# Performance work log

Hardware: AMD Instinct MI355X
Metric: run time of the kernel (lower is better)

The kernel has to match this reference:

```python
import jax, jax.numpy as jnp
import numpy as np

B, S, HID = 2, 2048, 1024
H, KVH = 16, 4           # query heads, kv heads
D = HID // H             # head_dim = 64
G = H // KVH             # group size (n_rep) = 4


def setup_inputs() -> dict:
    key = jax.random.key(0)
    ks = jax.random.split(key, 6)
    x = jax.random.normal(ks[0], (B, S, HID), dtype=jnp.float32)
    # RoPE tables: [S, D], standard theta=10000
    inv_freq = 1.0 / (10000.0 ** (jnp.arange(0, D, 2, dtype=jnp.float32) / D))
    freqs = jnp.arange(S, dtype=jnp.float32)[:, None] * inv_freq[None, :]  # [S, D/2]
    emb = jnp.concatenate([freqs, freqs], axis=-1)  # [S, D]
    cos, sin = jnp.cos(emb), jnp.sin(emb)
    scale = 0.02
    wq = jax.random.normal(ks[1], (HID, H * D), dtype=jnp.float32) * scale
    wk = jax.random.normal(ks[2], (HID, KVH * D), dtype=jnp.float32) * scale
    wv = jax.random.normal(ks[3], (HID, KVH * D), dtype=jnp.float32) * scale
    wo = jax.random.normal(ks[4], (H * D, HID), dtype=jnp.float32) * scale
    return {"x": x, "cos": cos, "sin": sin, "wq": wq, "wk": wk, "wv": wv, "wo": wo}


def _rotate_half(t):
    h = t.shape[-1] // 2
    return jnp.concatenate([-t[..., h:], t[..., :h]], axis=-1)


def reference(x, cos, sin, wq, wk, wv, wo):
    b, s, _ = x.shape
    q = (x @ wq).reshape(b, s, H, D)
    k = (x @ wk).reshape(b, s, KVH, D)
    v = (x @ wv).reshape(b, s, KVH, D)
    # RoPE (cos/sin broadcast over heads, unsqueeze_dim=1 -> [S,1,D])
    c = cos[:s, None, :]
    sn = sin[:s, None, :]
    q = q * c + _rotate_half(q) * sn
    k = k * c + _rotate_half(k) * sn
    # GQA attention without materializing repeated K/V: group q heads by kv head
    qg = q.reshape(b, s, KVH, G, D)
    scores = jnp.einsum('bqkgd,bskd->bkgqs', qg, k) / jnp.sqrt(jnp.asarray(D, q.dtype))
    causal = jnp.tril(jnp.ones((s, s), dtype=bool))  # [S_q, S_k]
    scores = jnp.where(causal[None, None, None, :, :], scores, -jnp.inf)
    p = jax.nn.softmax(scores, axis=-1)
    out = jnp.einsum('bkgqs,bskd->bqkgd', p, v).reshape(b, s, H * D)
    return out @ wo
```

## Files before the change

kernel.cpp:

```cpp
#include <hip/hip_runtime.h>
#include <hip/hip_bf16.h>


typedef short bfx8 __attribute__((ext_vector_type(8)));
typedef float fx4  __attribute__((ext_vector_type(4)));
typedef float fx16 __attribute__((ext_vector_type(16)));
typedef unsigned int ux4 __attribute__((ext_vector_type(4)));

#define DEV __device__ __forceinline__
#define ALPHA 0.18033688011112042f

DEV void load_lds16(const void* g, void* l) {
  __builtin_amdgcn_global_load_lds(
      (const __attribute__((address_space(1))) unsigned int*)g,
      (__attribute__((address_space(3))) unsigned int*)l, 16, 0, 0);
}

DEV unsigned short f2bf(float f) {
  unsigned int x = __builtin_bit_cast(unsigned int, f);
  unsigned int r = (x + 0x7fffu + ((x >> 16) & 1u)) >> 16;
  return (unsigned short)r;
}
DEV float bf2f(unsigned short u) {
  unsigned int x = ((unsigned int)u) << 16;
  return __builtin_bit_cast(float, x);
}
DEV float exp2_fast(float x) { float r; asm("v_exp_f32 %0, %1" : "=v"(r) : "v"(x)); return r; }
DEV unsigned cvtpk(float lo, float hi) {
  unsigned r; asm("v_cvt_pk_bf16_f32 %0, %1, %2" : "=v"(r) : "v"(lo), "v"(hi)); return r;
}


__global__ __launch_bounds__(256) void cvt_x_kernel(const float* __restrict__ x,
                                                    unsigned short* __restrict__ out) {
  int i = (blockIdx.x * 256 + threadIdx.x) * 8;
  fx4 a = *(const fx4*)(x + i);
  fx4 b = *(const fx4*)(x + i + 4);
  bfx8 r;
  r[0] = (short)f2bf(a[0]); r[1] = (short)f2bf(a[1]);
  r[2] = (short)f2bf(a[2]); r[3] = (short)f2bf(a[3]);
  r[4] = (short)f2bf(b[0]); r[5] = (short)f2bf(b[1]);
  r[6] = (short)f2bf(b[2]); r[7] = (short)f2bf(b[3]);
  *(bfx8*)(out + i) = r;
}


__global__ __launch_bounds__(256) void twqkv_kernel(const float* __restrict__ wq,
                                                    const float* __restrict__ wk,
                                                    const float* __restrict__ wv,
                                                    unsigned short* __restrict__ out) {
  __shared__ float tile[64 * 65];
  const int r0 = blockIdx.x * 64;
  const int c0 = blockIdx.y * 64;
  const float* src; int ncols, rofs;
  if (r0 < 1024)      { src = wq; ncols = 1024; rofs = r0; }
  else if (r0 < 1280) { src = wk; ncols = 256;  rofs = r0 - 1024; }
  else                { src = wv; ncols = 256;  rofs = r0 - 1280; }
  const int t = threadIdx.x;
#pragma unroll
  for (int p = 0; p < 4; ++p) {
    int idx = p * 256 + t;
    int cc = idx >> 4, q4 = idx & 15;
    fx4 v = *(const fx4*)(src + (size_t)(c0 + cc) * ncols + rofs + q4 * 4);
#pragma unroll
    for (int i = 0; i < 4; ++i) tile[(q4 * 4 + i) * 65 + cc] = v[i];
  }
  __syncthreads();
#pragma unroll
  for (int p = 0; p < 2; ++p) {
    int idx = p * 256 + t;
    int rr = idx >> 3, c8 = idx & 7;
    bfx8 v8;
#pragma unroll
    for (int i = 0; i < 8; ++i) v8[i] = (short)f2bf(tile[rr * 65 + c8 * 8 + i]);
    *(bfx8*)(out + (size_t)(r0 + rr) * 1024 + c0 + c8 * 8) = v8;
  }
}

__global__ __launch_bounds__(256) void two_kernel(const float* __restrict__ wo,
                                                  unsigned short* __restrict__ out) {
  __shared__ float tile[64 * 65];
  const int r0 = blockIdx.x * 64, c0 = blockIdx.y * 64;
  const int t = threadIdx.x;
#pragma unroll
  for (int p = 0; p < 4; ++p) {
    int idx = p * 256 + t;
    int cc = idx >> 4, q4 = idx & 15;
    fx4 v = *(const fx4*)(wo + (size_t)(c0 + cc) * 1024 + r0 + q4 * 4);
#pragma unroll
    for (int i = 0; i < 4; ++i) tile[(q4 * 4 + i) * 65 + cc] = v[i];
  }
  __syncthreads();
#pragma unroll
  for (int p = 0; p < 2; ++p) {
    int idx = p * 256 + t;
    int rr = idx >> 3, c8 = idx & 7;
    bfx8 v8;
#pragma unroll
    for (int i = 0; i < 8; ++i) v8[i] = (short)f2bf(tile[rr * 65 + c8 * 8 + i]);
    *(bfx8*)(out + (size_t)(r0 + rr) * 1024 + c0 + c8 * 8) = v8;
  }
}


__global__ __launch_bounds__(256) void vt_kernel(const unsigned short* __restrict__ qkv,
                                                 unsigned short* __restrict__ vT) {
  __shared__ __align__(16) unsigned short tile[64][72];
  const int sc = blockIdx.x;
  const int kvh = blockIdx.y, b = blockIdx.z;
  const int t = threadIdx.x;
  const unsigned short* src = qkv + ((size_t)b * 2048 + sc * 64) * 1536 + 1280 + kvh * 64;
#pragma unroll
  for (int p = 0; p < 2; ++p) {
    int idx = p * 256 + t;
    int row = idx >> 3, c = idx & 7;
    *(bfx8*)(&tile[row][c * 8]) = *(const bfx8*)(src + (size_t)row * 1536 + c * 8);
  }
  __syncthreads();
  unsigned short* dst = vT + ((size_t)(b * 4 + kvh) * 64) * 2048 + sc * 64;
#pragma unroll
  for (int p = 0; p < 2; ++p) {
    int idx = p * 256 + t;
    int d = idx >> 3, c = idx & 7;
    bfx8 v;
#pragma unroll
    for (int i = 0; i < 8; ++i) v[i] = (short)tile[c * 8 + i][d];
    *(bfx8*)(dst + (size_t)d * 2048 + c * 8) = v;
  }
}


template <bool OUT_BF16, bool FUSE_ROPE>
__global__ __launch_bounds__(256) void gemm_bt_kernel(const unsigned short* __restrict__ A,
                                                      const unsigned short* __restrict__ Bt,
                                                      void* __restrict__ Cp,
                                                      int M, int N, int K, int ldc,
                                                      const float* __restrict__ ct,
                                                      const float* __restrict__ st) {
  __shared__ __align__(16) unsigned short As[128 * 32];
  __shared__ __align__(16) unsigned short Bs[128 * 32];
  const int t = threadIdx.x;
  const int l = t & 63;
  const int w = t >> 6;
  const int wm = (w >> 1) * 64, wn = (w & 1) * 64;
  const int bm = blockIdx.x, bn = blockIdx.y;
  fx4 acc[4][4] = {};

  const int ra = t >> 2;
  const int ca = t & 3;

  for (int kt = 0; kt < K; kt += 32) {
    __syncthreads();
#pragma unroll
    for (int p = 0; p < 2; ++p) {
      int rr = ra + p * 64;
      int gca = ((ca ^ ((rr >> 1) & 3)) * 8);
      load_lds16(A + (size_t)(bm * 128 + rr) * K + kt + gca, (char*)As + p * 4096 + t * 16);
      load_lds16(Bt + (size_t)(bn * 128 + rr) * K + kt + gca, (char*)Bs + p * 4096 + t * 16);
    }
    __syncthreads();

    bfx8 af[4], bfr[4];
#pragma unroll
    for (int mi = 0; mi < 4; ++mi) {
      int row = wm + mi * 16 + (l & 15);
      int ch = (l >> 4) ^ ((row >> 1) & 3);
      af[mi] = *(const bfx8*)(As + row * 32 + ch * 8);
      int rowb = wn + mi * 16 + (l & 15);
      int chb = (l >> 4) ^ ((rowb >> 1) & 3);
      bfr[mi] = *(const bfx8*)(Bs + rowb * 32 + chb * 8);
    }
#pragma unroll
    for (int mi = 0; mi < 4; ++mi)
#pragma unroll
      for (int ni = 0; ni < 4; ++ni)
        acc[mi][ni] = __builtin_amdgcn_mfma_f32_16x16x32_bf16(af[mi], bfr[ni], acc[mi][ni], 0, 0, 0);
  }

  const int colbase = bn * 128 + wn;
  if (FUSE_ROPE && colbase < 1280) {
    const float qsc = (colbase < 1024) ? ALPHA : 1.0f;
    unsigned short* Cb = (unsigned short*)Cp;
#pragma unroll
    for (int mi = 0; mi < 4; ++mi) {
      int row0 = bm * 128 + wm + mi * 16 + (l >> 4) * 4;
#pragma unroll
      for (int r = 0; r < 4; ++r) {
        int row = row0 + r, s = row & 2047;
#pragma unroll
        for (int ni = 0; ni < 2; ++ni) {
          int d = ni * 16 + (l & 15);
          float c = ct[s * 64 + d], sn = st[s * 64 + d];
          float x0 = acc[mi][ni][r], x1 = acc[mi][ni + 2][r];
          Cb[(size_t)row * ldc + colbase + d]      = f2bf((x0 * c - x1 * sn) * qsc);
          Cb[(size_t)row * ldc + colbase + d + 32] = f2bf((x1 * c + x0 * sn) * qsc);
        }
      }
    }
  } else {
#pragma unroll
    for (int mi = 0; mi < 4; ++mi) {
      int row0 = bm * 128 + wm + mi * 16 + (l >> 4) * 4;
#pragma unroll
      for (int ni = 0; ni < 4; ++ni) {
        int col = colbase + ni * 16 + (l & 15);
#pragma unroll
        for (int r = 0; r < 4; ++r) {
          if (OUT_BF16)
            ((unsigned short*)Cp)[(size_t)(row0 + r) * ldc + col] = f2bf(acc[mi][ni][r]);
          else
            ((float*)Cp)[(size_t)(row0 + r) * ldc + col] = acc[mi][ni][r];
        }
      }
    }
  }
}


struct Frag { bfx8 kf[4]; bfx8 vf[4]; };

__global__ __launch_bounds__(64) void attn_kernel(const unsigned short* __restrict__ qkv,
                                                  const unsigned short* __restrict__ vT,
                                                  unsigned short* __restrict__ out) {
  __shared__ unsigned Ost[32 * 33];
  const int fid = blockIdx.x;
  const int pid = fid & 31;
  const int uu = fid >> 5;
  const int head = uu & 15, b = uu >> 4;
  const int kvh = head >> 2;
  const int l = threadIdx.x, q5 = l & 31, h = l >> 5;
  const size_t bbase = (size_t)b * 2048;
  const unsigned short* base = qkv + bbase * 1536;
  const unsigned short* kptr = base + 1024 + kvh * 64 + (size_t)q5 * 1536 + 8 * h;
  const unsigned short* vptr = vT + ((size_t)(b * 4 + kvh) * 64 + q5) * 2048 + 8 * h;

  Frag fA, fB;

#define LOADF(F, KB) do {                                                        \
    const unsigned short* kq = kptr + (size_t)(KB) * (32 * 1536);                \
    F.kf[0] = *(const bfx8*)(kq);                                                \
    F.kf[1] = *(const bfx8*)(kq + 16);                                           \
    F.kf[2] = *(const bfx8*)(kq + 32);                                           \
    F.kf[3] = *(const bfx8*)(kq + 48);                                           \
    const unsigned short* vq = vptr + (KB) * 32;                                 \
    F.vf[0] = *(const bfx8*)(vq);                                                \
    F.vf[1] = *(const bfx8*)(vq + 32 * 2048);                                    \
    F.vf[2] = *(const bfx8*)(vq + 16);                                           \
    F.vf[3] = *(const bfx8*)(vq + 16 + 32 * 2048);                               \
  } while (0)

#define STEP(F, KB) do {                                                         \
    fx16 s = {};                                                                 \
    s = __builtin_amdgcn_mfma_f32_32x32x16_bf16(F.kf[0], qf[0], s, 0, 0, 0);     \
    s = __builtin_amdgcn_mfma_f32_32x32x16_bf16(F.kf[1], qf[1], s, 0, 0, 0);     \
    s = __builtin_amdgcn_mfma_f32_32x32x16_bf16(F.kf[2], qf[2], s, 0, 0, 0);     \
    s = __builtin_amdgcn_mfma_f32_32x32x16_bf16(F.kf[3], qf[3], s, 0, 0, 0);     \
    if ((KB) == Tp) {                                                            \
      _Pragma("unroll")                                                          \
      for (int r = 0; r < 16; ++r) {                                             \
        int kr = (r & 3) + 8 * (r >> 2) + 4 * h;                                 \
        if (kr > q5) s[r] = -1e30f;                                              \
      }                                                                          \
    }                                                                            \
    float pmax = s[0];                                                           \
    _Pragma("unroll")                                                            \
    for (int r = 1; r < 16; ++r) pmax = fmaxf(pmax, s[r]);                       \
    pmax = fmaxf(pmax, __shfl_xor(pmax, 32, 64));                                \
    if (!__all(pmax <= mrun + 8.0f)) {                                           \
      float mnew = fmaxf(mrun, pmax);                                            \
      float corr = exp2_fast(mrun - mnew);                                       \
      mrun = mnew;                                                               \
      lrun *= corr;                                                              \
      o[0] *= corr; o[1] *= corr;                                                \
    }                                                                            \
    float lt = 0.f;                                                              \
    _Pragma("unroll")                                                            \
    for (int r = 0; r < 16; ++r) { float pv = exp2_fast(s[r] - mrun); s[r] = pv; lt += pv; } \
    lt += __shfl_xor(lt, 32, 64);                                                \
    lrun += lt;                                                                  \
    unsigned U[8];                                                               \
    _Pragma("unroll")                                                            \
    for (int k8 = 0; k8 < 8; ++k8) U[k8] = cvtpk(s[2 * k8], s[2 * k8 + 1]);      \
    _Pragma("unroll")                                                            \
    for (int kc = 0; kc < 2; ++kc) {                                             \
      unsigned send0 = h ? U[4 * kc] : U[4 * kc + 2];                            \
      unsigned send1 = h ? U[4 * kc + 1] : U[4 * kc + 3];                        \
      unsigned r0 = (unsigned)__shfl_xor((int)send0, 32, 64);                    \
      unsigned r1 = (unsigned)__shfl_xor((int)send1, 32, 64);                    \
      unsigned k0 = h ? U[4 * kc + 2] : U[4 * kc];                               \
      unsigned k1 = h ? U[4 * kc + 3] : U[4 * kc + 1];                           \
      ux4 fr;                                                                    \
      fr[0] = h ? r0 : k0; fr[1] = h ? r1 : k1;                                  \
      fr[2] = h ? k0 : r0; fr[3] = h ? k1 : r1;                                  \
      bfx8 pf = __builtin_bit_cast(bfx8, fr);                                    \
      o[0] = __builtin_amdgcn_mfma_f32_32x32x16_bf16(F.vf[kc * 2], pf, o[0], 0, 0, 0);     \
      o[1] = __builtin_amdgcn_mfma_f32_32x32x16_bf16(F.vf[kc * 2 + 1], pf, o[1], 0, 0, 0); \
    }                                                                            \
  } while (0)

#pragma unroll 1
  for (int sel = 0; sel < 2; ++sel) {
    const int Tp = sel ? (63 - pid) : pid;
    const int q0 = Tp * 32;
    const int nkb = Tp + 1;

    bfx8 qf[4];
#pragma unroll
    for (int dd = 0; dd < 4; ++dd)
      qf[dd] = *(const bfx8*)(base + (size_t)(q0 + q5) * 1536 + head * 64 + dd * 16 + 8 * h);

    fx16 o[2] = {};
    float mrun = -1e30f, lrun = 0.f;

    LOADF(fA, 0);
    int kb = 0;
    while (true) {
      if (kb + 1 < nkb) LOADF(fB, kb + 1);
      STEP(fA, kb);
      ++kb; if (kb >= nkb) break;
      if (kb + 1 < nkb) LOADF(fA, kb + 1);
      STEP(fB, kb);
      ++kb; if (kb >= nkb) break;
    }

    __syncthreads();
    float inv = 1.0f / lrun;
#pragma unroll
    for (int dt = 0; dt < 2; ++dt)
#pragma unroll
      for (int rp = 0; rp < 8; ++rp) {
        int r = 2 * rp;
        float a = o[dt][r] * inv, bb = o[dt][r + 1] * inv;
        int d = 32 * dt + (r & 3) + 8 * (r >> 2) + 4 * h;
        Ost[q5 * 33 + (d >> 1)] = cvtpk(a, bb);
      }
    __syncthreads();
    {
      int rr = l >> 1, half = l & 1;
      const unsigned* src = Ost + rr * 33 + half * 16;
      unsigned short* dst = out + (bbase + q0 + rr) * 1024 + head * 64 + half * 32;
#pragma unroll
      for (int u2 = 0; u2 < 4; ++u2) {
        ux4 v4;
        v4[0] = src[4 * u2]; v4[1] = src[4 * u2 + 1];
        v4[2] = src[4 * u2 + 2]; v4[3] = src[4 * u2 + 3];
        *(ux4*)(dst + u2 * 8) = v4;
      }
    }
  }
#undef LOADF
#undef STEP
}


extern "C" void kernel_launch(void* const* d_in, const int* in_sizes, int n_in,
                              void* d_out, int out_size, void* d_ws, size_t ws_size,
                              hipStream_t stream) {
  const float* x    = (const float*)d_in[0];
  const float* cosb = (const float*)d_in[1];
  const float* sinb = (const float*)d_in[2];
  const float* wq   = (const float*)d_in[3];
  const float* wk   = (const float*)d_in[4];
  const float* wv   = (const float*)d_in[5];
  const float* wo   = (const float*)d_in[6];
  float* out = (float*)d_out;

  char* ws = (char*)d_ws;
  unsigned short* xb    = (unsigned short*)ws;
  unsigned short* attn  = (unsigned short*)ws;
  unsigned short* wqkvT = (unsigned short*)(ws + 8388608);
  unsigned short* vT    = (unsigned short*)(ws + 8388608);
  unsigned short* woT   = (unsigned short*)(ws + 11534336);
  unsigned short* qkv   = (unsigned short*)(ws + 13631488);

  cvt_x_kernel<<<2048, 256, 0, stream>>>(x, xb);
  twqkv_kernel<<<dim3(24, 16), 256, 0, stream>>>(wq, wk, wv, wqkvT);
  two_kernel<<<dim3(16, 16), 256, 0, stream>>>(wo, woT);
  gemm_bt_kernel<true, true><<<dim3(32, 12), 256, 0, stream>>>(xb, wqkvT, qkv, 4096, 1536, 1024, 1536, cosb, sinb);
  vt_kernel<<<dim3(32, 4, 2), 256, 0, stream>>>(qkv, vT);
  attn_kernel<<<1024, 64, 0, stream>>>(qkv, vT, attn);
  gemm_bt_kernel<false, false><<<dim3(32, 8), 256, 0, stream>>>(attn, woT, out, 4096, 1024, 1024, 1024, nullptr, nullptr);
}
```

Before: 210.2 us.

## Split attention KV loop across two waves and merge weight-transpose kernels

The attention kernel now runs two wavefronts per block. Each wave processes alternating key blocks with triple-buffered fragment loads, and the partial softmax states (max, sum, output) are merged through shared memory before the output is written. This is meant to double the parallelism per query tile and shorten the serial KV loop, at the cost of extra LDS traffic, barriers and a combine step. Separately, the Q/K/V and O weight transpose kernels are fused into one launch to save a kernel launch.

```diff
diff --git a/kernel.cpp b/kernel.cpp
--- a/kernel.cpp
+++ b/kernel.cpp
@@ -45,17 +45,24 @@
 }
 
 
-__global__ __launch_bounds__(256) void twqkv_kernel(const float* __restrict__ wq,
-                                                    const float* __restrict__ wk,
-                                                    const float* __restrict__ wv,
-                                                    unsigned short* __restrict__ out) {
+__global__ __launch_bounds__(256) void tw_kernel(const float* __restrict__ wq,
+                                                 const float* __restrict__ wk,
+                                                 const float* __restrict__ wv,
+                                                 const float* __restrict__ wo,
+                                                 unsigned short* __restrict__ wqkvT,
+                                                 unsigned short* __restrict__ woT) {
   __shared__ float tile[64 * 65];
-  const int r0 = blockIdx.x * 64;
+  const int bx = blockIdx.x;
   const int c0 = blockIdx.y * 64;
-  const float* src; int ncols, rofs;
-  if (r0 < 1024)      { src = wq; ncols = 1024; rofs = r0; }
-  else if (r0 < 1280) { src = wk; ncols = 256;  rofs = r0 - 1024; }
-  else                { src = wv; ncols = 256;  rofs = r0 - 1280; }
+  const float* src; int ncols, rofs, r0; unsigned short* dst;
+  if (bx < 24) {
+    r0 = bx * 64; dst = wqkvT;
+    if (r0 < 1024)      { src = wq; ncols = 1024; rofs = r0; }
+    else if (r0 < 1280) { src = wk; ncols = 256;  rofs = r0 - 1024; }
+    else                { src = wv; ncols = 256;  rofs = r0 - 1280; }
+  } else {
+    r0 = (bx - 24) * 64; dst = woT; src = wo; ncols = 1024; rofs = r0;
+  }
   const int t = threadIdx.x;
 #pragma unroll
   for (int p = 0; p < 4; ++p) {
@@ -73,32 +80,7 @@
     bfx8 v8;
 #pragma unroll
     for (int i = 0; i < 8; ++i) v8[i] = (short)f2bf(tile[rr * 65 + c8 * 8 + i]);
-    *(bfx8*)(out + (size_t)(r0 + rr) * 1024 + c0 + c8 * 8) = v8;
-  }
-}
-
-__global__ __launch_bounds__(256) void two_kernel(const float* __restrict__ wo,
-                                                  unsigned short* __restrict__ out) {
-  __shared__ float tile[64 * 65];
-  const int r0 = blockIdx.x * 64, c0 = blockIdx.y * 64;
-  const int t = threadIdx.x;
-#pragma unroll
-  for (int p = 0; p < 4; ++p) {
-    int idx = p * 256 + t;
-    int cc = idx >> 4, q4 = idx & 15;
-    fx4 v = *(const fx4*)(wo + (size_t)(c0 + cc) * 1024 + r0 + q4 * 4);
-#pragma unroll
-    for (int i = 0; i < 4; ++i) tile[(q4 * 4 + i) * 65 + cc] = v[i];
-  }
-  __syncthreads();
-#pragma unroll
-  for (int p = 0; p < 2; ++p) {
-    int idx = p * 256 + t;
-    int rr = idx >> 3, c8 = idx & 7;
-    bfx8 v8;
-#pragma unroll
-    for (int i = 0; i < 8; ++i) v8[i] = (short)f2bf(tile[rr * 65 + c8 * 8 + i]);
-    *(bfx8*)(out + (size_t)(r0 + rr) * 1024 + c0 + c8 * 8) = v8;
+    *(bfx8*)(dst + (size_t)(r0 + rr) * 1024 + c0 + c8 * 8) = v8;
   }
 }
 
@@ -219,22 +201,25 @@
 
 struct Frag { bfx8 kf[4]; bfx8 vf[4]; };
 
-__global__ __launch_bounds__(64) void attn_kernel(const unsigned short* __restrict__ qkv,
-                                                  const unsigned short* __restrict__ vT,
-                                                  unsigned short* __restrict__ out) {
+__global__ __launch_bounds__(128) void attn_kernel(const unsigned short* __restrict__ qkv,
+                                                   const unsigned short* __restrict__ vT,
+                                                   unsigned short* __restrict__ out) {
+  __shared__ float OX[2][16][64];
   __shared__ unsigned Ost[32 * 33];
+  __shared__ float Msh[2 * 64], Lsh[2 * 64];
   const int fid = blockIdx.x;
   const int pid = fid & 31;
   const int uu = fid >> 5;
   const int head = uu & 15, b = uu >> 4;
   const int kvh = head >> 2;
-  const int l = threadIdx.x, q5 = l & 31, h = l >> 5;
+  const int t = threadIdx.x, w = t >> 6, l = t & 63;
+  const int q5 = l & 31, h = l >> 5;
   const size_t bbase = (size_t)b * 2048;
   const unsigned short* base = qkv + bbase * 1536;
   const unsigned short* kptr = base + 1024 + kvh * 64 + (size_t)q5 * 1536 + 8 * h;
   const unsigned short* vptr = vT + ((size_t)(b * 4 + kvh) * 64 + q5) * 2048 + 8 * h;
 
-  Frag fA, fB;
+  Frag fA, fB, fC;
 
 #define LOADF(F, KB) do {                                                        \
     const unsigned short* kq = kptr + (size_t)(KB) * (32 * 1536);                \
@@ -312,41 +297,60 @@
     fx16 o[2] = {};
     float mrun = -1e30f, lrun = 0.f;
 
-    LOADF(fA, 0);
-    int kb = 0;
-    while (true) {
-      if (kb + 1 < nkb) LOADF(fB, kb + 1);
-      STEP(fA, kb);
-      ++kb; if (kb >= nkb) break;
-      if (kb + 1 < nkb) LOADF(fA, kb + 1);
-      STEP(fB, kb);
-      ++kb; if (kb >= nkb) break;
-    }
-
-    __syncthreads();
-    float inv = 1.0f / lrun;
-#pragma unroll
-    for (int dt = 0; dt < 2; ++dt)
-#pragma unroll
-      for (int rp = 0; rp < 8; ++rp) {
-        int r = 2 * rp;
-        float a = o[dt][r] * inv, bb = o[dt][r + 1] * inv;
-        int d = 32 * dt + (r & 3) + 8 * (r >> 2) + 4 * h;
-        Ost[q5 * 33 + (d >> 1)] = cvtpk(a, bb);
+    int kb = w;
+    if (kb < nkb) {
+      LOADF(fA, kb);
+      if (kb + 2 < nkb) LOADF(fB, kb + 2);
+      while (true) {
+        if (kb + 4 < nkb) LOADF(fC, kb + 4);
+        STEP(fA, kb);
+        kb += 2; if (kb >= nkb) break;
+        if (kb + 4 < nkb) LOADF(fA, kb + 4);
+        STEP(fB, kb);
+        kb += 2; if (kb >= nkb) break;
+        if (kb + 4 < nkb) LOADF(fB, kb + 4);
+        STEP(fC, kb);
+        kb += 2; if (kb >= nkb) break;
       }
-    __syncthreads();
+    }
+
+    Msh[w * 64 + l] = mrun;
+    __syncthreads();
+    float mtot = fmaxf(Msh[l], Msh[64 + l]);
+    float sc = exp2_fast(mrun - mtot);
+    Lsh[w * 64 + l] = lrun * sc;
+    o[0] *= sc; o[1] *= sc;
     {
-      int rr = l >> 1, half = l & 1;
-      const unsigned* src = Ost + rr * 33 + half * 16;
-      unsigned short* dst = out + (bbase + q0 + rr) * 1024 + head * 64 + half * 32;
-#pragma unroll
-      for (int u2 = 0; u2 < 4; ++u2) {
-        ux4 v4;
-        v4[0] = src[4 * u2]; v4[1] = src[4 * u2 + 1];
-        v4[2] = src[4 * u2 + 2]; v4[3] = src[4 * u2 + 3];
-        *(ux4*)(dst + u2 * 8) = v4;
-      }
-    }
+      fx16 oth = w ? o[0] : o[1];
+      int dto = 1 - w;
+#pragma unroll
+      for (int r = 0; r < 16; ++r) OX[dto][r][l] = oth[r];
+    }
+    __syncthreads();
+    float ltot = Lsh[l] + Lsh[64 + l];
+    float inv = 1.0f / ltot;
+    fx16 mine = w ? o[1] : o[0];
+#pragma unroll
+    for (int r = 0; r < 16; ++r) mine[r] = (mine[r] + OX[w][r][l]) * inv;
+
+#pragma unroll
+    for (int rp = 0; rp < 8; ++rp) {
+      int r = 2 * rp;
+      int d = 32 * w + (r & 3) + 8 * (r >> 2) + 4 * h;
+      Ost[q5 * 33 + (d >> 1)] = cvtpk(mine[r], mine[r + 1]);
+    }
+    __syncthreads();
+    {
+      int q = t >> 2, c = t & 3;
+      const unsigned* src = Ost + q * 33 + c * 8;
+      unsigned short* dst = out + (bbase + q0 + q) * 1024 + head * 64 + c * 16;
+      ux4 v0, v1;
+      v0[0] = src[0]; v0[1] = src[1]; v0[2] = src[2]; v0[3] = src[3];
+      v1[0] = src[4]; v1[1] = src[5]; v1[2] = src[6]; v1[3] = src[7];
+      *(ux4*)(dst) = v0;
+      *(ux4*)(dst + 8) = v1;
+    }
+    __syncthreads();
   }
 #undef LOADF
 #undef STEP
@@ -374,10 +378,9 @@
   unsigned short* qkv   = (unsigned short*)(ws + 13631488);
 
   cvt_x_kernel<<<2048, 256, 0, stream>>>(x, xb);
-  twqkv_kernel<<<dim3(24, 16), 256, 0, stream>>>(wq, wk, wv, wqkvT);
-  two_kernel<<<dim3(16, 16), 256, 0, stream>>>(wo, woT);
+  tw_kernel<<<dim3(40, 16), 256, 0, stream>>>(wq, wk, wv, wo, wqkvT, woT);
   gemm_bt_kernel<true, true><<<dim3(32, 12), 256, 0, stream>>>(xb, wqkvT, qkv, 4096, 1536, 1024, 1536, cosb, sinb);
   vt_kernel<<<dim3(32, 4, 2), 256, 0, stream>>>(qkv, vT);
-  attn_kernel<<<1024, 64, 0, stream>>>(qkv, vT, attn);
+  attn_kernel<<<1024, 128, 0, stream>>>(qkv, vT, attn);
   gemm_bt_kernel<false, false><<<dim3(32, 8), 256, 0, stream>>>(attn, woT, out, 4096, 1024, 1024, 1024, nullptr, nullptr);
 }
```

After: 216.8 us. 1.03x slower.
